# Kernel optimization log

Measured on AMD Instinct MI355X. Metric: run time of the kernel, lower is better.

The kernel has to match this reference:

```python
import jax, jax.numpy as jnp
import numpy as np

N, E = 100000, 1600000
NF, HC, NC = 32, 64, 64


def setup_inputs() -> dict:
    key = jax.random.key(0)
    ks = jax.random.split(key, 12)
    s = 0.05
    return {
        "x": jax.random.normal(ks[0], (N, NF), dtype=jnp.float32),
        "edge_index": jax.random.randint(ks[1], (2, E), 0, N, dtype=jnp.int64),
        "eps1": jnp.float32(0.0),
        "eps2": jnp.float32(0.0),
        "W1a": jax.random.normal(ks[2], (NF, HC), dtype=jnp.float32) * s,
        "b1a": jnp.zeros((HC,), dtype=jnp.float32),
        "W1b": jax.random.normal(ks[3], (HC, HC), dtype=jnp.float32) * s,
        "b1b": jnp.zeros((HC,), dtype=jnp.float32),
        "W2a": jax.random.normal(ks[4], (HC, HC), dtype=jnp.float32) * s,
        "b2a": jnp.zeros((HC,), dtype=jnp.float32),
        "W2b": jax.random.normal(ks[5], (HC, NC), dtype=jnp.float32) * s,
        "b2b": jnp.zeros((NC,), dtype=jnp.float32),
    }


def _gin_conv(h, src, dst, eps, Wa, ba, Wb, bb, num_nodes):
    # sum-aggregate neighbor features: out[dst] += h[src]
    agg = jax.ops.segment_sum(h[src], dst, num_segments=num_nodes)
    z = (1.0 + eps) * h + agg
    # 2-layer MLP: Linear -> ReLU -> Linear
    z = jax.nn.relu(z @ Wa + ba)
    return z @ Wb + bb


def reference(x, edge_index, eps1, eps2, W1a, b1a, W1b, b1b, W2a, b2a, W2b, b2b):
    src, dst = edge_index[0], edge_index[1]
    n = x.shape[0]
    emb = _gin_conv(x, src, dst, eps1, W1a, b1a, W1b, b1b, n)  # [N, HC]
    h = jax.nn.relu(emb)  # dropout is identity in eval mode
    logits = _gin_conv(h, src, dst, eps2, W2a, b2a, W2b, b2b, n)  # [N, NC]
    return (logits, emb)
```

## Files before the change

kernel.cpp:

```cpp
#include <hip/hip_runtime.h>


#define NFEAT 32
#define HID   64
#define NCLS  64

#define BSH   9
#define BNODES 512
#define NBKT_MAX 256
#define BCAP  16384
#define ECAP  2048

typedef unsigned int uint;
typedef unsigned short ushortT;
typedef __attribute__((ext_vector_type(8))) short bf16x8;
typedef __attribute__((ext_vector_type(4))) float f32x4;

__device__ __forceinline__ int clampi(int v, int hi){ v = v < 0 ? 0 : v; return v > hi ? hi : v; }

__device__ __forceinline__ ushortT f2b(float f){
  uint u = __float_as_uint(f);
  u = (u + 0x7FFFu + ((u >> 16) & 1u)) >> 16;
  return (ushortT)u;
}
__device__ __forceinline__ float b2f_lo(uint u){ return __uint_as_float(u << 16); }
__device__ __forceinline__ float b2f_hi(uint u){ return __uint_as_float(u & 0xFFFF0000u); }
__device__ __forceinline__ uint pack2(float lo, float hi){
  return (uint)f2b(lo) | ((uint)f2b(hi) << 16);
}


__global__ void k_prep(const float* __restrict__ x, ushortT* __restrict__ xb, int n4,
                       const float* __restrict__ W1a, const float* __restrict__ W1b,
                       const float* __restrict__ W2a, const float* __restrict__ W2b,
                       ushortT* __restrict__ T1a, ushortT* __restrict__ T1b,
                       ushortT* __restrict__ T2a, ushortT* __restrict__ T2b,
                       int* __restrict__ bktCnt, int nbkt){
  int t = blockIdx.x*256 + threadIdx.x;
  if (t < n4){
    float4 v = reinterpret_cast<const float4*>(x)[t];
    ushort4 o = { f2b(v.x), f2b(v.y), f2b(v.z), f2b(v.w) };
    reinterpret_cast<ushort4*>(xb)[t] = o;
  }
  if (t < nbkt) bktCnt[t] = 0;
  if (t < 14336){
    const float* W; ushortT* T; int K; int base;
    if      (t <  2048){ W=W1a; T=T1a; K=32; base=0;     }
    else if (t <  6144){ W=W1b; T=T1b; K=64; base=2048;  }
    else if (t < 10240){ W=W2a; T=T2a; K=64; base=6144;  }
    else               { W=W2b; T=T2b; K=64; base=10240; }
    int o = t - base;
    int k = o >> 6, c = o & 63;
    T[c*K + k] = f2b(W[o]);
  }
}


__global__ void k_bucket(const int* __restrict__ src, const int* __restrict__ dst,
                         int E, int N, int nbkt,
                         int* __restrict__ bktCnt, int* __restrict__ bktData){
  __shared__ int s_cnt[NBKT_MAX];
  __shared__ int s_base[NBKT_MAX];
  const int t = threadIdx.x;
  for (int j = t; j < nbkt; j += 256) s_cnt[j] = 0;
  __syncthreads();

  const int e0 = blockIdx.x * 4096;
  const int e1 = min(e0 + 4096, E);
  for (int e = e0 + t; e < e1; e += 256){
    int d = clampi(dst[e], N-1);
    atomicAdd(&s_cnt[d >> BSH], 1);
  }
  __syncthreads();
  for (int j = t; j < nbkt; j += 256){
    int c = s_cnt[j];
    s_base[j] = (c > 0) ? atomicAdd(&bktCnt[j], c) : 0;
    s_cnt[j] = 0;
  }
  __syncthreads();
  for (int e = e0 + t; e < e1; e += 256){
    int d = clampi(dst[e], N-1);
    int s = clampi(src[e], N-1);
    int b = d >> BSH;
    int p = s_base[b] + atomicAdd(&s_cnt[b], 1);
    if (p < BCAP)
      bktData[(size_t)b * BCAP + p] = ((d & (BNODES-1)) << 17) | s;
  }
}


__global__ __launch_bounds__(BNODES)
void k_build(const int* __restrict__ bktCnt, const int* __restrict__ bktData,
             int nbkt, int* __restrict__ rowptr, int* __restrict__ eidx, int N){
  __shared__ int s_bs[NBKT_MAX];
  __shared__ int s_h[BNODES];
  __shared__ int s_cur[BNODES];
  const int b = blockIdx.x, t = threadIdx.x;

  if (t < NBKT_MAX) s_bs[t] = (t < nbkt) ? min(bktCnt[t], BCAP) : 0;
  __syncthreads();
  for (int off = 1; off < NBKT_MAX; off <<= 1){
    int add = 0;
    if (t < NBKT_MAX && t >= off) add = s_bs[t-off];
    __syncthreads();
    if (t < NBKT_MAX) s_bs[t] += add;
    __syncthreads();
  }
  const int cnt  = min(bktCnt[b], BCAP);
  const int base = s_bs[b] - cnt;
  if (b == 0 && t == 0) rowptr[N] = s_bs[nbkt-1];
  const int* __restrict__ data = bktData + (size_t)b * BCAP;

  s_h[t] = 0;
  __syncthreads();
  for (int e = t; e < cnt; e += BNODES) atomicAdd(&s_h[data[e] >> 17], 1);
  __syncthreads();

  int deg = s_h[t];
  for (int off = 1; off < BNODES; off <<= 1){
    int add = (t >= off) ? s_h[t-off] : 0;
    __syncthreads();
    s_h[t] += add;
    __syncthreads();
  }
  int excl = s_h[t] - deg;
  int node = b * BNODES + t;
  if (node < N) rowptr[node] = base + excl;
  s_cur[t] = excl;
  __syncthreads();

  for (int e = t; e < cnt; e += BNODES){
    int val = data[e];
    int d = val >> 17;
    int p = atomicAdd(&s_cur[d], 1);
    eidx[base + p] = val & 0x1FFFF;
  }
}


template<int K, bool WRITE_HB>
__global__ __launch_bounds__(512)
void k_fused(const uint4* __restrict__ f4,
             const int* __restrict__ rowptr, const int* __restrict__ eidx,
             const float* __restrict__ epsP,
             const ushortT* __restrict__ WaT,
             const float* __restrict__ ba,
             const ushortT* __restrict__ WbT,
             const float* __restrict__ bb,
             float* __restrict__ out,
             ushortT* __restrict__ hb, int N){
  constexpr int RS = K/8;
  constexpr int CH = RS/4;
  constexpr int U  = (CH == 1) ? 8 : 4;
  constexpr int ZS = K + 8;
  constexpr int HS = 72;
  __shared__ int s_row[65];
  __shared__ int s_eidx[ECAP];
  __shared__ __align__(16) ushortT zt[64*ZS];
  __shared__ __align__(16) ushortT ht[64*HS];
  const int t = threadIdx.x;
  const int row0 = blockIdx.x * 64;

  const int e0 = rowptr[min(row0, N)];
  const int e1 = rowptr[min(row0 + 64, N)];
  if (t < 65){
    int idx = row0 + t; if (idx > N) idx = N;
    s_row[t] = rowptr[idx];
  }
  const int cnt = e1 - e0;
  for (int j = t; j < cnt && j < ECAP; j += 512) s_eidx[j] = eidx[e0 + j];
  __syncthreads();

  {
    const int n = t >> 3;
    const int L = t & 7;
    const int q = L & 3;
    const int s = L >> 2;
    const int node = row0 + n;
    float acc[CH*8];
    #pragma unroll
    for (int j = 0; j < CH*8; ++j) acc[j] = 0.f;

    const int b    = s_row[n] - e0;
    const int e    = s_row[n+1] - e0;
    const int iend = min(e, ECAP);
    for (int i = b + s; i < iend; i += 2*U){
      float m[U]; int src[U];
      #pragma unroll
      for (int u = 0; u < U; ++u){
        int ii = i + 2*u;
        m[u]   = (ii < iend) ? 1.f : 0.f;
        src[u] = s_eidx[min(ii, iend-1)];
      }
      uint4 v[U][CH];
      #pragma unroll
      for (int u = 0; u < U; ++u)
        #pragma unroll
        for (int c = 0; c < CH; ++c)
          v[u][c] = f4[(size_t)src[u]*RS + q*CH + c];
      #pragma unroll
      for (int u = 0; u < U; ++u)
        #pragma unroll
        for (int c = 0; c < CH; ++c){
          acc[c*8+0] = fmaf(m[u], b2f_lo(v[u][c].x), acc[c*8+0]);
          acc[c*8+1] = fmaf(m[u], b2f_hi(v[u][c].x), acc[c*8+1]);
          acc[c*8+2] = fmaf(m[u], b2f_lo(v[u][c].y), acc[c*8+2]);
          acc[c*8+3] = fmaf(m[u], b2f_hi(v[u][c].y), acc[c*8+3]);
          acc[c*8+4] = fmaf(m[u], b2f_lo(v[u][c].z), acc[c*8+4]);
          acc[c*8+5] = fmaf(m[u], b2f_hi(v[u][c].z), acc[c*8+5]);
          acc[c*8+6] = fmaf(m[u], b2f_lo(v[u][c].w), acc[c*8+6]);
          acc[c*8+7] = fmaf(m[u], b2f_hi(v[u][c].w), acc[c*8+7]);
        }
    }
    {
      int rem = iend - (b + s);
      int i2  = (rem > 0) ? (b + s + ((rem + 1) & ~1)) : (b + s);
      for (; i2 < e; i2 += 2){
        int src0 = eidx[e0 + i2];
        #pragma unroll
        for (int c = 0; c < CH; ++c){
          uint4 v = f4[(size_t)src0*RS + q*CH + c];
          acc[c*8+0] += b2f_lo(v.x); acc[c*8+1] += b2f_hi(v.x);
          acc[c*8+2] += b2f_lo(v.y); acc[c*8+3] += b2f_hi(v.y);
          acc[c*8+4] += b2f_lo(v.z); acc[c*8+5] += b2f_hi(v.z);
          acc[c*8+6] += b2f_lo(v.w); acc[c*8+7] += b2f_hi(v.w);
        }
      }
    }
    if (s == 1 && node < N){
      const float se = 1.0f + epsP[0];
      #pragma unroll
      for (int c = 0; c < CH; ++c){
        uint4 v = f4[(size_t)node*RS + q*CH + c];
        acc[c*8+0] = fmaf(se, b2f_lo(v.x), acc[c*8+0]);
        acc[c*8+1] = fmaf(se, b2f_hi(v.x), acc[c*8+1]);
        acc[c*8+2] = fmaf(se, b2f_lo(v.y), acc[c*8+2]);
        acc[c*8+3] = fmaf(se, b2f_hi(v.y), acc[c*8+3]);
        acc[c*8+4] = fmaf(se, b2f_lo(v.z), acc[c*8+4]);
        acc[c*8+5] = fmaf(se, b2f_hi(v.z), acc[c*8+5]);
        acc[c*8+6] = fmaf(se, b2f_lo(v.w), acc[c*8+6]);
        acc[c*8+7] = fmaf(se, b2f_hi(v.w), acc[c*8+7]);
      }
    }
    #pragma unroll
    for (int j = 0; j < CH*8; ++j) acc[j] += __shfl_xor(acc[j], 4);
    if (s == 0){
      #pragma unroll
      for (int c = 0; c < CH; ++c){
        uint4 z;
        z.x = pack2(acc[c*8+0], acc[c*8+1]);
        z.y = pack2(acc[c*8+2], acc[c*8+3]);
        z.z = pack2(acc[c*8+4], acc[c*8+5]);
        z.w = pack2(acc[c*8+6], acc[c*8+7]);
        *reinterpret_cast<uint4*>(&zt[n*ZS + (q*CH + c)*8]) = z;
      }
    }
  }
  __syncthreads();

  const int w  = t >> 6;
  const int l  = t & 63;
  const int lr = l & 15;
  const int lg = l >> 4;
  const int rf = w & 3;
  const int c0 = (w >> 2) * 2;
  f32x4 c1[2];
  #pragma unroll
  for (int cl = 0; cl < 2; ++cl){ float bv = ba[(c0+cl)*16 + lr]; c1[cl] = (f32x4){bv,bv,bv,bv}; }
  #pragma unroll
  for (int kf = 0; kf < K/32; ++kf){
    bf16x8 a = *reinterpret_cast<const bf16x8*>(&zt[(rf*16 + lr)*ZS + kf*32 + lg*8]);
    #pragma unroll
    for (int cl = 0; cl < 2; ++cl){
      bf16x8 bfr = *reinterpret_cast<const bf16x8*>(&WaT[((c0+cl)*16 + lr)*K + kf*32 + lg*8]);
      c1[cl] = __builtin_amdgcn_mfma_f32_16x16x32_bf16(a, bfr, c1[cl], 0, 0, 0);
    }
  }
  #pragma unroll
  for (int cl = 0; cl < 2; ++cl)
    #pragma unroll
    for (int r = 0; r < 4; ++r)
      ht[(rf*16 + lg*4 + r)*HS + (c0+cl)*16 + lr] = f2b(fmaxf(c1[cl][r], 0.f));
  __syncthreads();

  f32x4 c2[2];
  #pragma unroll
  for (int cl = 0; cl < 2; ++cl){ float bv = bb[(c0+cl)*16 + lr]; c2[cl] = (f32x4){bv,bv,bv,bv}; }
  #pragma unroll
  for (int kf = 0; kf < 2; ++kf){
    bf16x8 a = *reinterpret_cast<const bf16x8*>(&ht[(rf*16 + lr)*HS + kf*32 + lg*8]);
    #pragma unroll
    for (int cl = 0; cl < 2; ++cl){
      bf16x8 bfr = *reinterpret_cast<const bf16x8*>(&WbT[((c0+cl)*16 + lr)*64 + kf*32 + lg*8]);
      c2[cl] = __builtin_amdgcn_mfma_f32_16x16x32_bf16(a, bfr, c2[cl], 0, 0, 0);
    }
  }
  #pragma unroll
  for (int cl = 0; cl < 2; ++cl)
    #pragma unroll
    for (int r = 0; r < 4; ++r){
      int row = row0 + rf*16 + lg*4 + r;
      if (row < N){
        float v = c2[cl][r];
        out[(size_t)row*64 + (c0+cl)*16 + lr] = v;
        if (WRITE_HB) hb[(size_t)row*64 + (c0+cl)*16 + lr] = f2b(fmaxf(v, 0.f));
      }
    }
}


extern "C" void kernel_launch(void* const* d_in, const int* in_sizes, int n_in,
                              void* d_out, int out_size, void* d_ws, size_t ws_size,
                              hipStream_t stream) {
  const int N = in_sizes[0] / NFEAT;
  const int E = in_sizes[1] / 2;
  const int nbkt = (N + BNODES - 1) / BNODES;

  const float* x    = (const float*)d_in[0];
  const int*   ei   = (const int*)d_in[1];
  const int*   srcI = ei;
  const int*   dstI = ei + E;
  const float* eps1 = (const float*)d_in[2];
  const float* eps2 = (const float*)d_in[3];
  const float* W1a  = (const float*)d_in[4];
  const float* b1a  = (const float*)d_in[5];
  const float* W1b  = (const float*)d_in[6];
  const float* b1b  = (const float*)d_in[7];
  const float* W2a  = (const float*)d_in[8];
  const float* b2a  = (const float*)d_in[9];
  const float* W2b  = (const float*)d_in[10];
  const float* b2b  = (const float*)d_in[11];

  float* outLogits = (float*)d_out;
  float* outEmb    = outLogits + (size_t)N * HID;

  char* w = (char*)d_ws;
  size_t off = 0;
  auto alloc = [&](size_t bytes) -> void* {
    void* p = w + off;
    off = (off + bytes + 255) & ~(size_t)255;
    return p;
  };
  int*     rowptr  = (int*)alloc((size_t)(N+1) * sizeof(int));
  int*     eidx    = (int*)alloc((size_t)E * sizeof(int));
  int*     bktCnt  = (int*)alloc((size_t)NBKT_MAX * sizeof(int));
  ushortT* T1a     = (ushortT*)alloc(64*32*sizeof(ushortT));
  ushortT* T1b     = (ushortT*)alloc(64*64*sizeof(ushortT));
  ushortT* T2a     = (ushortT*)alloc(64*64*sizeof(ushortT));
  ushortT* T2b     = (ushortT*)alloc(64*64*sizeof(ushortT));
  int*     bktData = (int*)alloc((size_t)NBKT_MAX * BCAP * sizeof(int));
  ushortT* xb      = (ushortT*)alloc((size_t)N * NFEAT * sizeof(ushortT));
  ushortT* hb      = (ushortT*)alloc((size_t)N * HID * sizeof(ushortT));

  const int n4 = N * NFEAT / 4;
  k_prep<<<(n4+255)/256, 256, 0, stream>>>(x, xb, n4, W1a, W1b, W2a, W2b,
                                           T1a, T1b, T2a, T2b, bktCnt, nbkt);

  k_bucket<<<(E+4095)/4096, 256, 0, stream>>>(srcI, dstI, E, N, nbkt, bktCnt, bktData);
  k_build <<<nbkt, BNODES, 0, stream>>>(bktCnt, bktData, nbkt, rowptr, eidx, N);

  const int nblk = (N + 63) / 64;
  k_fused<NFEAT, true><<<nblk, 512, 0, stream>>>((const uint4*)xb, rowptr, eidx,
      eps1, T1a, b1a, T1b, b1b, outEmb, hb, N);

  k_fused<HID, false><<<nblk, 512, 0, stream>>>((const uint4*)hb, rowptr, eidx,
      eps2, T2a, b2a, T2b, b2b, outLogits, (ushortT*)nullptr, N);
}
```

Baseline: 133.2 us.

## Split gather from MLP and slice features into column-major chunks for cache locality

```diff
diff --git a/kernel.cpp b/kernel.cpp
--- a/kernel.cpp
+++ b/kernel.cpp
@@ -30,17 +30,20 @@
 }
 
 
-__global__ void k_prep(const float* __restrict__ x, ushortT* __restrict__ xb, int n4,
+__global__ void k_prep(const float* __restrict__ x, uint4* __restrict__ xb4, int N,
                        const float* __restrict__ W1a, const float* __restrict__ W1b,
                        const float* __restrict__ W2a, const float* __restrict__ W2b,
                        ushortT* __restrict__ T1a, ushortT* __restrict__ T1b,
                        ushortT* __restrict__ T2a, ushortT* __restrict__ T2b,
                        int* __restrict__ bktCnt, int nbkt){
   int t = blockIdx.x*256 + threadIdx.x;
-  if (t < n4){
-    float4 v = reinterpret_cast<const float4*>(x)[t];
-    ushort4 o = { f2b(v.x), f2b(v.y), f2b(v.z), f2b(v.w) };
-    reinterpret_cast<ushort4*>(xb)[t] = o;
+  if (t < N*4){
+    int n = t >> 2, s = t & 3;
+    const float* xr = x + (size_t)n*NFEAT + s*8;
+    uint4 o;
+    o.x = pack2(xr[0], xr[1]); o.y = pack2(xr[2], xr[3]);
+    o.z = pack2(xr[4], xr[5]); o.w = pack2(xr[6], xr[7]);
+    xb4[(size_t)s*N + n] = o;
   }
   if (t < nbkt) bktCnt[t] = 0;
   if (t < 14336){
@@ -138,28 +141,20 @@
 }
 
 
-template<int K, bool WRITE_HB>
-__global__ __launch_bounds__(512)
-void k_fused(const uint4* __restrict__ f4,
-             const int* __restrict__ rowptr, const int* __restrict__ eidx,
-             const float* __restrict__ epsP,
-             const ushortT* __restrict__ WaT,
-             const float* __restrict__ ba,
-             const ushortT* __restrict__ WbT,
-             const float* __restrict__ bb,
-             float* __restrict__ out,
-             ushortT* __restrict__ hb, int N){
-  constexpr int RS = K/8;
-  constexpr int CH = RS/4;
-  constexpr int U  = (CH == 1) ? 8 : 4;
-  constexpr int ZS = K + 8;
-  constexpr int HS = 72;
+template<int K>
+__global__ __launch_bounds__(256)
+void k_gath(const uint4* __restrict__ tb,
+            const int* __restrict__ rowptr, const int* __restrict__ eidx,
+            const float* __restrict__ epsP, ushortT* __restrict__ z, int N){
+  constexpr int QL     = (K/4)/8;
+  constexpr int SPLITW = 4/QL;
+  constexpr int U      = 4;
   __shared__ int s_row[65];
   __shared__ int s_eidx[ECAP];
-  __shared__ __align__(16) ushortT zt[64*ZS];
-  __shared__ __align__(16) ushortT ht[64*HS];
-  const int t = threadIdx.x;
-  const int row0 = blockIdx.x * 64;
+  const int t    = threadIdx.x;
+  const int tile = blockIdx.x >> 2;
+  const int sl   = blockIdx.x & 3;
+  const int row0 = tile * 64;
 
   const int e0 = rowptr[min(row0, N)];
   const int e1 = rowptr[min(row0 + 64, N)];
@@ -168,95 +163,94 @@
     s_row[t] = rowptr[idx];
   }
   const int cnt = e1 - e0;
-  for (int j = t; j < cnt && j < ECAP; j += 512) s_eidx[j] = eidx[e0 + j];
-  __syncthreads();
-
+  for (int j = t; j < cnt && j < ECAP; j += 256) s_eidx[j] = eidx[e0 + j];
+  __syncthreads();
+
+  const int n  = t >> 2;
+  const int L  = t & 3;
+  const int q  = (SPLITW == 4) ? 0 : (L >> 1);
+  const int sp = L & (SPLITW - 1);
+  const int node = row0 + n;
+  const uint4* __restrict__ tbq = tb + (size_t)sl * N * QL + q;
+
+  float acc[8];
+  #pragma unroll
+  for (int j = 0; j < 8; ++j) acc[j] = 0.f;
+
+  if (sp == 0 && node < N){
+    const float se = 1.0f + epsP[0];
+    uint4 v = tbq[(size_t)node * QL];
+    acc[0] = se * b2f_lo(v.x); acc[1] = se * b2f_hi(v.x);
+    acc[2] = se * b2f_lo(v.y); acc[3] = se * b2f_hi(v.y);
+    acc[4] = se * b2f_lo(v.z); acc[5] = se * b2f_hi(v.z);
+    acc[6] = se * b2f_lo(v.w); acc[7] = se * b2f_hi(v.w);
+  }
+
+  const int b    = s_row[n] - e0;
+  const int e    = s_row[n+1] - e0;
+  const int iend = min(e, ECAP);
+  for (int i = b + sp; i < iend; i += SPLITW*U){
+    float m[U]; int src[U];
+    #pragma unroll
+    for (int u = 0; u < U; ++u){
+      int ii = i + u*SPLITW;
+      m[u]   = (ii < iend) ? 1.f : 0.f;
+      src[u] = s_eidx[min(ii, iend-1)];
+    }
+    uint4 v[U];
+    #pragma unroll
+    for (int u = 0; u < U; ++u) v[u] = tbq[(size_t)src[u] * QL];
+    #pragma unroll
+    for (int u = 0; u < U; ++u){
+      acc[0] = fmaf(m[u], b2f_lo(v[u].x), acc[0]);
+      acc[1] = fmaf(m[u], b2f_hi(v[u].x), acc[1]);
+      acc[2] = fmaf(m[u], b2f_lo(v[u].y), acc[2]);
+      acc[3] = fmaf(m[u], b2f_hi(v[u].y), acc[3]);
+      acc[4] = fmaf(m[u], b2f_lo(v[u].z), acc[4]);
+      acc[5] = fmaf(m[u], b2f_hi(v[u].z), acc[5]);
+      acc[6] = fmaf(m[u], b2f_lo(v[u].w), acc[6]);
+      acc[7] = fmaf(m[u], b2f_hi(v[u].w), acc[7]);
+    }
+  }
   {
-    const int n = t >> 3;
-    const int L = t & 7;
-    const int q = L & 3;
-    const int s = L >> 2;
-    const int node = row0 + n;
-    float acc[CH*8];
-    #pragma unroll
-    for (int j = 0; j < CH*8; ++j) acc[j] = 0.f;
-
-    const int b    = s_row[n] - e0;
-    const int e    = s_row[n+1] - e0;
-    const int iend = min(e, ECAP);
-    for (int i = b + s; i < iend; i += 2*U){
-      float m[U]; int src[U];
-      #pragma unroll
-      for (int u = 0; u < U; ++u){
-        int ii = i + 2*u;
-        m[u]   = (ii < iend) ? 1.f : 0.f;
-        src[u] = s_eidx[min(ii, iend-1)];
-      }
-      uint4 v[U][CH];
-      #pragma unroll
-      for (int u = 0; u < U; ++u)
-        #pragma unroll
-        for (int c = 0; c < CH; ++c)
-          v[u][c] = f4[(size_t)src[u]*RS + q*CH + c];
-      #pragma unroll
-      for (int u = 0; u < U; ++u)
-        #pragma unroll
-        for (int c = 0; c < CH; ++c){
-          acc[c*8+0] = fmaf(m[u], b2f_lo(v[u][c].x), acc[c*8+0]);
-          acc[c*8+1] = fmaf(m[u], b2f_hi(v[u][c].x), acc[c*8+1]);
-          acc[c*8+2] = fmaf(m[u], b2f_lo(v[u][c].y), acc[c*8+2]);
-          acc[c*8+3] = fmaf(m[u], b2f_hi(v[u][c].y), acc[c*8+3]);
-          acc[c*8+4] = fmaf(m[u], b2f_lo(v[u][c].z), acc[c*8+4]);
-          acc[c*8+5] = fmaf(m[u], b2f_hi(v[u][c].z), acc[c*8+5]);
-          acc[c*8+6] = fmaf(m[u], b2f_lo(v[u][c].w), acc[c*8+6]);
-          acc[c*8+7] = fmaf(m[u], b2f_hi(v[u][c].w), acc[c*8+7]);
-        }
-    }
-    {
-      int rem = iend - (b + s);
-      int i2  = (rem > 0) ? (b + s + ((rem + 1) & ~1)) : (b + s);
-      for (; i2 < e; i2 += 2){
-        int src0 = eidx[e0 + i2];
-        #pragma unroll
-        for (int c = 0; c < CH; ++c){
-          uint4 v = f4[(size_t)src0*RS + q*CH + c];
-          acc[c*8+0] += b2f_lo(v.x); acc[c*8+1] += b2f_hi(v.x);
-          acc[c*8+2] += b2f_lo(v.y); acc[c*8+3] += b2f_hi(v.y);
-          acc[c*8+4] += b2f_lo(v.z); acc[c*8+5] += b2f_hi(v.z);
-          acc[c*8+6] += b2f_lo(v.w); acc[c*8+7] += b2f_hi(v.w);
-        }
-      }
-    }
-    if (s == 1 && node < N){
-      const float se = 1.0f + epsP[0];
-      #pragma unroll
-      for (int c = 0; c < CH; ++c){
-        uint4 v = f4[(size_t)node*RS + q*CH + c];
-        acc[c*8+0] = fmaf(se, b2f_lo(v.x), acc[c*8+0]);
-        acc[c*8+1] = fmaf(se, b2f_hi(v.x), acc[c*8+1]);
-        acc[c*8+2] = fmaf(se, b2f_lo(v.y), acc[c*8+2]);
-        acc[c*8+3] = fmaf(se, b2f_hi(v.y), acc[c*8+3]);
-        acc[c*8+4] = fmaf(se, b2f_lo(v.z), acc[c*8+4]);
-        acc[c*8+5] = fmaf(se, b2f_hi(v.z), acc[c*8+5]);
-        acc[c*8+6] = fmaf(se, b2f_lo(v.w), acc[c*8+6]);
-        acc[c*8+7] = fmaf(se, b2f_hi(v.w), acc[c*8+7]);
-      }
-    }
-    #pragma unroll
-    for (int j = 0; j < CH*8; ++j) acc[j] += __shfl_xor(acc[j], 4);
-    if (s == 0){
-      #pragma unroll
-      for (int c = 0; c < CH; ++c){
-        uint4 z;
-        z.x = pack2(acc[c*8+0], acc[c*8+1]);
-        z.y = pack2(acc[c*8+2], acc[c*8+3]);
-        z.z = pack2(acc[c*8+4], acc[c*8+5]);
-        z.w = pack2(acc[c*8+6], acc[c*8+7]);
-        *reinterpret_cast<uint4*>(&zt[n*ZS + (q*CH + c)*8]) = z;
-      }
-    }
-  }
-  __syncthreads();
+    int i2 = b + sp;
+    if (iend > i2) i2 += ((iend - i2 + SPLITW - 1)/SPLITW)*SPLITW;
+    for (; i2 < e; i2 += SPLITW){
+      int s0 = eidx[e0 + i2];
+      uint4 v = tbq[(size_t)s0 * QL];
+      acc[0] += b2f_lo(v.x); acc[1] += b2f_hi(v.x);
+      acc[2] += b2f_lo(v.y); acc[3] += b2f_hi(v.y);
+      acc[4] += b2f_lo(v.z); acc[5] += b2f_hi(v.z);
+      acc[6] += b2f_lo(v.w); acc[7] += b2f_hi(v.w);
+    }
+  }
+  #pragma unroll
+  for (int o = 1; o < SPLITW; o <<= 1)
+    #pragma unroll
+    for (int j = 0; j < 8; ++j) acc[j] += __shfl_xor(acc[j], o);
+
+  if (sp == 0 && node < N){
+    uint4 o;
+    o.x = pack2(acc[0], acc[1]); o.y = pack2(acc[2], acc[3]);
+    o.z = pack2(acc[4], acc[5]); o.w = pack2(acc[6], acc[7]);
+    reinterpret_cast<uint4*>(z)[(size_t)node*(K/8) + sl*QL + q] = o;
+  }
+}
+
+
+template<int K, bool WRITE_HB4>
+__global__ __launch_bounds__(512)
+void k_mlp(const ushortT* __restrict__ z,
+           const ushortT* __restrict__ WaT,
+           const float* __restrict__ ba,
+           const ushortT* __restrict__ WbT,
+           const float* __restrict__ bb,
+           float* __restrict__ out,
+           ushortT* __restrict__ hb4, int N){
+  constexpr int HS = 72;
+  __shared__ __align__(16) ushortT ht[64*HS];
+  const int t = threadIdx.x;
+  const int row0 = blockIdx.x * 64;
 
   const int w  = t >> 6;
   const int l  = t & 63;
@@ -264,12 +258,13 @@
   const int lg = l >> 4;
   const int rf = w & 3;
   const int c0 = (w >> 2) * 2;
+
   f32x4 c1[2];
   #pragma unroll
   for (int cl = 0; cl < 2; ++cl){ float bv = ba[(c0+cl)*16 + lr]; c1[cl] = (f32x4){bv,bv,bv,bv}; }
   #pragma unroll
   for (int kf = 0; kf < K/32; ++kf){
-    bf16x8 a = *reinterpret_cast<const bf16x8*>(&zt[(rf*16 + lr)*ZS + kf*32 + lg*8]);
+    bf16x8 a = *reinterpret_cast<const bf16x8*>(&z[(size_t)(row0 + rf*16 + lr)*K + kf*32 + lg*8]);
     #pragma unroll
     for (int cl = 0; cl < 2; ++cl){
       bf16x8 bfr = *reinterpret_cast<const bf16x8*>(&WaT[((c0+cl)*16 + lr)*K + kf*32 + lg*8]);
@@ -302,8 +297,12 @@
       int row = row0 + rf*16 + lg*4 + r;
       if (row < N){
         float v = c2[cl][r];
-        out[(size_t)row*64 + (c0+cl)*16 + lr] = v;
-        if (WRITE_HB) hb[(size_t)row*64 + (c0+cl)*16 + lr] = f2b(fmaxf(v, 0.f));
+        int col = (c0+cl)*16 + lr;
+        out[(size_t)row*64 + col] = v;
+        if (WRITE_HB4){
+          int s2 = col >> 4, f = col & 15;
+          hb4[(size_t)s2*N*16 + (size_t)row*16 + f] = f2b(fmaxf(v, 0.f));
+        }
       }
     }
 }
@@ -314,7 +313,9 @@
                               hipStream_t stream) {
   const int N = in_sizes[0] / NFEAT;
   const int E = in_sizes[1] / 2;
-  const int nbkt = (N + BNODES - 1) / BNODES;
+  const int nbkt  = (N + BNODES - 1) / BNODES;
+  const int ntile = (N + 63) / 64;
+  const int NP    = ntile * 64;
 
   const float* x    = (const float*)d_in[0];
   const int*   ei   = (const int*)d_in[1];
@@ -348,21 +349,25 @@
   ushortT* T1b     = (ushortT*)alloc(64*64*sizeof(ushortT));
   ushortT* T2a     = (ushortT*)alloc(64*64*sizeof(ushortT));
   ushortT* T2b     = (ushortT*)alloc(64*64*sizeof(ushortT));
-  int*     bktData = (int*)alloc((size_t)NBKT_MAX * BCAP * sizeof(int));
-  ushortT* xb      = (ushortT*)alloc((size_t)N * NFEAT * sizeof(ushortT));
-  ushortT* hb      = (ushortT*)alloc((size_t)N * HID * sizeof(ushortT));
-
-  const int n4 = N * NFEAT / 4;
-  k_prep<<<(n4+255)/256, 256, 0, stream>>>(x, xb, n4, W1a, W1b, W2a, W2b,
+  size_t ubytes = (size_t)NBKT_MAX * BCAP * sizeof(int);
+  size_t zbytes = (size_t)NP * (NFEAT + HID) * sizeof(ushortT);
+  char*  ublk   = (char*)alloc(ubytes > zbytes ? ubytes : zbytes);
+  int*     bktData = (int*)ublk;
+  ushortT* z1b     = (ushortT*)ublk;
+  ushortT* z2b     = (ushortT*)(ublk + (size_t)NP*NFEAT*2);
+  uint4*   xb4     = (uint4*)alloc((size_t)4 * N * 16);
+  ushortT* hb4     = (ushortT*)alloc((size_t)4 * N * 16 * sizeof(ushortT));
+
+  const int np = N * 4;
+  k_prep<<<(np+255)/256, 256, 0, stream>>>(x, xb4, N, W1a, W1b, W2a, W2b,
                                            T1a, T1b, T2a, T2b, bktCnt, nbkt);
 
   k_bucket<<<(E+4095)/4096, 256, 0, stream>>>(srcI, dstI, E, N, nbkt, bktCnt, bktData);
   k_build <<<nbkt, BNODES, 0, stream>>>(bktCnt, bktData, nbkt, rowptr, eidx, N);
 
-  const int nblk = (N + 63) / 64;
-  k_fused<NFEAT, true><<<nblk, 512, 0, stream>>>((const uint4*)xb, rowptr, eidx,
-      eps1, T1a, b1a, T1b, b1b, outEmb, hb, N);
-
-  k_fused<HID, false><<<nblk, 512, 0, stream>>>((const uint4*)hb, rowptr, eidx,
-      eps2, T2a, b2a, T2b, b2b, outLogits, (ushortT*)nullptr, N);
-}
+  k_gath<NFEAT><<<ntile*4, 256, 0, stream>>>(xb4, rowptr, eidx, eps1, z1b, N);
+  k_mlp<NFEAT, true><<<ntile, 512, 0, stream>>>(z1b, T1a, b1a, T1b, b1b, outEmb, hb4, N);
+
+  k_gath<HID><<<ntile*4, 256, 0, stream>>>((const uint4*)hb4, rowptr, eidx, eps2, z2b, N);
+  k_mlp<HID, false><<<ntile, 512, 0, stream>>>(z2b, T2a, b2a, T2b, b2b, outLogits, (ushortT*)nullptr, N);
+}
```

New measurement: 160.7 us. 20.6% more time.
